# Kernel tuning notes

Measured on AMD Instinct MI355X. Metric: run time of the kernel, lower is better.

The kernel has to match this reference:

```python
import jax, jax.numpy as jnp
import numpy as np

B, H, W_, D, K = 64, 28, 28, 512, 32


def setup_inputs() -> dict:
    key = jax.random.key(0)
    k1, k2, k3 = jax.random.split(key, 3)
    x = jax.random.normal(k1, (B, H, W_, D), dtype=jnp.float32)
    # 1x1 conv weight, no bias: [D_in, K] (he_normal-like scale)
    W = jax.random.normal(k2, (D, K), dtype=jnp.float32) * np.sqrt(2.0 / D)
    # cluster offset tensor C (original shape (1,1,1,512,32), squeezed to [D,K])
    C = jax.random.normal(k3, (D, K), dtype=jnp.float32) * np.sqrt(2.0 / D)
    return {"x": x, "W": W, "C": C}


def reference(x, W, C):
    # 1x1 conv == per-pixel matmul: [B,H,W,D] @ [D,K] -> [B,H,W,K]
    s = jnp.einsum('bhwd,dk->bhwk', x, W)
    a = jax.nn.softmax(s, axis=-1)  # soft cluster assignment
    # Original math: v[b,d,k] = sum_{h,w} a[b,h,w,k] * (x[b,h,w,d] + C[d,k])
    # Algebraically identical split avoids the [B,H,W,D,K] 5D intermediate:
    #   sum_hw a*x  (matmul of assignments with features)
    # + (sum_hw a) * C  (cheap correction term)
    v = jnp.einsum('bhwk,bhwd->bdk', a, x) + jnp.sum(a, axis=(1, 2))[:, None, :] * C[None]
    return v.reshape(v.shape[0], -1)  # flatten -> [B, D*K]
```

## Files before the change

kernel.cpp:

```cpp
#include <hip/hip_runtime.h>

#define NB 64
#define HW 784
#define DD 512
#define KK 32
#define BPB 14
#define PPB 56
#define CHUNK 32
#define NCHUNK 2

typedef __attribute__((ext_vector_type(8))) short bf16x8;
typedef __attribute__((ext_vector_type(4))) float f32x4;

#define PART_F   ((size_t)NB * BPB * 4 * 16 * 64 * 4)
#define ASUM_OFF PART_F
#define WS_NEED  ((PART_F + (size_t)NB * BPB * KK) * sizeof(float))

__device__ __forceinline__ unsigned short f2bf(float f) {
    unsigned u = __float_as_uint(f);
    u += 0x7fffu + ((u >> 16) & 1u);
    return (unsigned short)(u >> 16);
}

template <bool USE_WS>
__global__ __launch_bounds__(256, 2) void netvlad_stage1(
    const float* __restrict__ x, const float* __restrict__ Wg,
    const float* __restrict__ Cg, float* __restrict__ out,
    float* __restrict__ ws)
{
    __shared__ __align__(16) unsigned short xs[CHUNK * 520];
    __shared__ float spart[4][CHUNK][33];
    __shared__ __align__(16) unsigned short aTe[KK * 40];
    __shared__ float ared[8][KK];
    __shared__ float asumF[KK];

    const int tid = threadIdx.x;
    const int l   = tid & 63, w = tid >> 6;
    const int l15 = l & 15,  lq = l >> 4;
    const int k   = tid & 31, pg = tid >> 5;
    const int bid = blockIdx.x;
    const int b   = bid / BPB;
    const int pb  = (bid % BPB) * PPB;
    const float* xb = x + (size_t)b * HW * DD;

    bf16x8 Wf[4][2];
#pragma unroll
    for (int ks = 0; ks < 4; ++ks)
#pragma unroll
        for (int nt = 0; nt < 2; ++nt)
#pragma unroll
            for (int j = 0; j < 8; ++j)
                Wf[ks][nt][j] = (short)f2bf(Wg[(w*128 + ks*32 + lq*8 + j) * KK + nt*16 + l15]);

    f32x4 acc[2][8];
#pragma unroll
    for (int mt = 0; mt < 2; ++mt)
#pragma unroll
        for (int nt = 0; nt < 8; ++nt)
#pragma unroll
            for (int jj = 0; jj < 4; ++jj) acc[mt][nt][jj] = 0.f;
    float asum_part = 0.f;

    auto stageChunk = [&](int c) {
#pragma unroll
        for (int h = 0; h < 2; ++h) {
            float4 r[8];
#pragma unroll
            for (int j = 0; j < 8; ++j) {
                const int f = tid + 256*(h*8 + j), row = f >> 7, c4 = f & 127;
                const int p = c*CHUNK + row;
                const int gp = pb + (p < PPB ? p : PPB - 1);
                r[j] = *(const float4*)(xb + (size_t)gp * DD + c4*4);
            }
#pragma unroll
            for (int j = 0; j < 8; ++j) {
                const int f = tid + 256*(h*8 + j), row = f >> 7, c4 = f & 127;
                uint2 pk = make_uint2((unsigned)f2bf(r[j].x) | ((unsigned)f2bf(r[j].y) << 16),
                                      (unsigned)f2bf(r[j].z) | ((unsigned)f2bf(r[j].w) << 16));
                *(uint2*)&xs[row*520 + c4*4] = pk;
            }
        }
    };

    stageChunk(0);
    __syncthreads();

    for (int c = 0; c < NCHUNK; ++c) {
        f32x4 sp[2][2];
#pragma unroll
        for (int mt = 0; mt < 2; ++mt)
#pragma unroll
            for (int nt = 0; nt < 2; ++nt)
#pragma unroll
                for (int jj = 0; jj < 4; ++jj) sp[mt][nt][jj] = 0.f;
#pragma unroll
        for (int ks = 0; ks < 4; ++ks) {
            bf16x8 af[2];
#pragma unroll
            for (int mt = 0; mt < 2; ++mt)
                af[mt] = *(const bf16x8*)&xs[(mt*16 + l15)*520 + w*128 + ks*32 + lq*8];
#pragma unroll
            for (int mt = 0; mt < 2; ++mt)
#pragma unroll
                for (int nt = 0; nt < 2; ++nt)
                    sp[mt][nt] = __builtin_amdgcn_mfma_f32_16x16x32_bf16(
                        af[mt], Wf[ks][nt], sp[mt][nt], 0, 0, 0);
        }
#pragma unroll
        for (int mt = 0; mt < 2; ++mt)
#pragma unroll
            for (int nt = 0; nt < 2; ++nt)
#pragma unroll
                for (int jj = 0; jj < 4; ++jj)
                    spart[w][mt*16 + lq*4 + jj][nt*16 + l15] = sp[mt][nt][jj];
        __syncthreads();

        const int valid = (PPB - c*CHUNK < CHUNK) ? (PPB - c*CHUNK) : CHUNK;
#pragma unroll
        for (int i = 0; i < 4; ++i) {
            const int p = pg + 8*i;
            const float s = spart[0][p][k] + spart[1][p][k]
                          + spart[2][p][k] + spart[3][p][k];
            const float e = __expf(s);
            float su = e;
#pragma unroll
            for (int msk = 16; msk >= 1; msk >>= 1)
                su += __shfl_xor(su, msk);
            const float a = (p < valid) ? e / su : 0.f;
            asum_part += a;
            aTe[k*40 + p] = f2bf(a);
        }
        __syncthreads();

        bf16x8 afr[2];
#pragma unroll
        for (int mt = 0; mt < 2; ++mt)
            afr[mt] = *(const bf16x8*)&aTe[(mt*16 + l15)*40 + lq*8];
#pragma unroll
        for (int nt = 0; nt < 8; ++nt) {
            const int d = w*128 + nt*16 + l15;
            bf16x8 bfr;
#pragma unroll
            for (int j = 0; j < 8; ++j) {
                const int jj = (j + 2*lq) & 7;
                bfr[jj] = (short)xs[(lq*8 + jj)*520 + d];
            }
#pragma unroll
            for (int mt = 0; mt < 2; ++mt)
                acc[mt][nt] = __builtin_amdgcn_mfma_f32_16x16x32_bf16(
                    afr[mt], bfr, acc[mt][nt], 0, 0, 0);
        }
        __syncthreads();

        if (c + 1 < NCHUNK) {
            stageChunk(c + 1);
            __syncthreads();
        }
    }

    ared[pg][k] = asum_part;
    __syncthreads();
    if (tid < KK) {
        float s = 0.f;
#pragma unroll
        for (int g = 0; g < 8; ++g) s += ared[g][tid];
        if (USE_WS) ws[ASUM_OFF + (size_t)bid * KK + tid] = s;
        else        asumF[tid] = s;
    }

    if (USE_WS) {
        float4* o = (float4*)ws + ((size_t)bid * 4 + w) * (16 * 64);
#pragma unroll
        for (int mt = 0; mt < 2; ++mt)
#pragma unroll
            for (int nt = 0; nt < 8; ++nt)
                o[(mt*8 + nt)*64 + l] = make_float4(acc[mt][nt][0], acc[mt][nt][1],
                                                    acc[mt][nt][2], acc[mt][nt][3]);
    } else {
        __syncthreads();
        float* ob = out + (size_t)b * (DD * KK);
#pragma unroll
        for (int mt = 0; mt < 2; ++mt)
#pragma unroll
            for (int nt = 0; nt < 8; ++nt)
#pragma unroll
                for (int jj = 0; jj < 4; ++jj) {
                    const int kk = mt*16 + lq*4 + jj;
                    const int d  = w*128 + nt*16 + l15;
                    atomicAdd(&ob[d*KK + kk], acc[mt][nt][jj] + asumF[kk] * Cg[d*KK + kk]);
                }
    }
}

__global__ __launch_bounds__(256) void netvlad_stage2(
    const float* __restrict__ ws, const float* __restrict__ Cg,
    float* __restrict__ out)
{
    __shared__ float lds[128 * 33];
    __shared__ float asumT[KK];

    const int t = threadIdx.x;
    const int b = blockIdx.x >> 2;
    const int w = blockIdx.x & 3;

    if (t < KK) {
        float s = 0.f;
#pragma unroll
        for (int p = 0; p < BPB; ++p)
            s += ws[ASUM_OFF + (size_t)(b*BPB + p) * KK + t];
        asumT[t] = s;
    }

    const float4* wsp = (const float4*)ws;
    float4 v[4];
#pragma unroll
    for (int i = 0; i < 4; ++i) v[i] = make_float4(0.f, 0.f, 0.f, 0.f);
    for (int p = 0; p < BPB; ++p) {
        const size_t base = ((size_t)(b*BPB + p) * 4 + w) * (16 * 64);
#pragma unroll
        for (int i = 0; i < 4; ++i) {
            const float4 f4 = wsp[base + t + 256*i];
            v[i].x += f4.x; v[i].y += f4.y; v[i].z += f4.z; v[i].w += f4.w;
        }
    }
#pragma unroll
    for (int i = 0; i < 4; ++i) {
        const int flat = t + 256*i;
        const int f = flat >> 6, lane = flat & 63;
        const int mt = f >> 3, nt = f & 7;
        const int q = lane >> 4, r15 = lane & 15;
        const int dl = nt*16 + r15;
        const int kb = mt*16 + q*4;
        lds[dl*33 + kb + 0] = v[i].x;
        lds[dl*33 + kb + 1] = v[i].y;
        lds[dl*33 + kb + 2] = v[i].z;
        lds[dl*33 + kb + 3] = v[i].w;
    }
    __syncthreads();

    float* outw = out + (size_t)b * (DD*KK) + w * 128 * KK;
    const float* Cw = Cg + w * 128 * KK;
#pragma unroll
    for (int i = 0; i < 4; ++i) {
        const int o4 = t + 256*i;
        const int dl = o4 >> 3, kq = (o4 & 7) * 4;
        const float4 c4 = *(const float4*)&Cw[dl*KK + kq];
        float4 rr;
        rr.x = lds[dl*33 + kq + 0] + asumT[kq + 0] * c4.x;
        rr.y = lds[dl*33 + kq + 1] + asumT[kq + 1] * c4.y;
        rr.z = lds[dl*33 + kq + 2] + asumT[kq + 2] * c4.z;
        rr.w = lds[dl*33 + kq + 3] + asumT[kq + 3] * c4.w;
        ((float4*)outw)[o4] = rr;
    }
}

extern "C" void kernel_launch(void* const* d_in, const int* in_sizes, int n_in,
                              void* d_out, int out_size, void* d_ws, size_t ws_size,
                              hipStream_t stream) {
    const float* x = (const float*)d_in[0];
    const float* W = (const float*)d_in[1];
    const float* C = (const float*)d_in[2];
    float* out = (float*)d_out;

    if (ws_size >= WS_NEED) {
        float* ws = (float*)d_ws;
        netvlad_stage1<true><<<dim3(NB * BPB), dim3(256), 0, stream>>>(x, W, C, out, ws);
        netvlad_stage2<<<dim3(NB * 4), dim3(256), 0, stream>>>(ws, C, out);
    } else {
        hipMemsetAsync(out, 0, (size_t)out_size * sizeof(float), stream);
        netvlad_stage1<false><<<dim3(NB * BPB), dim3(256), 0, stream>>>(x, W, C, out, nullptr);
    }
}
```

Before: 58.12 us.

## Use single-chunk blocks of 28 pixels and store partials in bf16

```diff
diff --git a/kernel.cpp b/kernel.cpp
--- a/kernel.cpp
+++ b/kernel.cpp
@@ -4,34 +4,36 @@
 #define HW 784
 #define DD 512
 #define KK 32
-#define BPB 14
-#define PPB 56
-#define CHUNK 32
-#define NCHUNK 2
+#define BPB 28
+#define PPB 28
+#define SLOTS 32
 
 typedef __attribute__((ext_vector_type(8))) short bf16x8;
 typedef __attribute__((ext_vector_type(4))) float f32x4;
-
-#define PART_F   ((size_t)NB * BPB * 4 * 16 * 64 * 4)
-#define ASUM_OFF PART_F
-#define WS_NEED  ((PART_F + (size_t)NB * BPB * KK) * sizeof(float))
+typedef __attribute__((ext_vector_type(4))) unsigned short u16x4;
+
+#define NBLK (NB * BPB)
+#define PART_BYTES ((size_t)NBLK * 4 * 16 * 64 * 8)
+#define WS_NEED    (PART_BYTES + (size_t)NBLK * KK * 4)
 
 __device__ __forceinline__ unsigned short f2bf(float f) {
     unsigned u = __float_as_uint(f);
     u += 0x7fffu + ((u >> 16) & 1u);
     return (unsigned short)(u >> 16);
 }
+__device__ __forceinline__ float bf2f(unsigned short u) {
+    return __uint_as_float((unsigned)u << 16);
+}
 
 template <bool USE_WS>
-__global__ __launch_bounds__(256, 2) void netvlad_stage1(
+__global__ __launch_bounds__(256) void netvlad_stage1(
     const float* __restrict__ x, const float* __restrict__ Wg,
     const float* __restrict__ Cg, float* __restrict__ out,
-    float* __restrict__ ws)
+    void* __restrict__ ws)
 {
-    __shared__ __align__(16) unsigned short xs[CHUNK * 520];
-    __shared__ float spart[4][CHUNK][33];
+    __shared__ __align__(16) unsigned short xs[SLOTS * 520];
+    __shared__ unsigned short spart[4][SLOTS][33];
     __shared__ __align__(16) unsigned short aTe[KK * 40];
-    __shared__ float ared[8][KK];
     __shared__ float asumF[KK];
 
     const int tid = threadIdx.x;
@@ -61,31 +63,26 @@
             for (int jj = 0; jj < 4; ++jj) acc[mt][nt][jj] = 0.f;
     float asum_part = 0.f;
 
-    auto stageChunk = [&](int c) {
-#pragma unroll
-        for (int h = 0; h < 2; ++h) {
-            float4 r[8];
-#pragma unroll
-            for (int j = 0; j < 8; ++j) {
-                const int f = tid + 256*(h*8 + j), row = f >> 7, c4 = f & 127;
-                const int p = c*CHUNK + row;
-                const int gp = pb + (p < PPB ? p : PPB - 1);
-                r[j] = *(const float4*)(xb + (size_t)gp * DD + c4*4);
-            }
-#pragma unroll
-            for (int j = 0; j < 8; ++j) {
-                const int f = tid + 256*(h*8 + j), row = f >> 7, c4 = f & 127;
-                uint2 pk = make_uint2((unsigned)f2bf(r[j].x) | ((unsigned)f2bf(r[j].y) << 16),
-                                      (unsigned)f2bf(r[j].z) | ((unsigned)f2bf(r[j].w) << 16));
-                *(uint2*)&xs[row*520 + c4*4] = pk;
-            }
-        }
-    };
-
-    stageChunk(0);
-    __syncthreads();
-
-    for (int c = 0; c < NCHUNK; ++c) {
+#pragma unroll
+    for (int h = 0; h < 2; ++h) {
+        float4 r[8];
+#pragma unroll
+        for (int j = 0; j < 8; ++j) {
+            const int f = tid + 256*(h*8 + j), row = f >> 7, c4 = f & 127;
+            const int gp = pb + (row < PPB ? row : PPB - 1);
+            r[j] = *(const float4*)(xb + (size_t)gp * DD + c4*4);
+        }
+#pragma unroll
+        for (int j = 0; j < 8; ++j) {
+            const int f = tid + 256*(h*8 + j), row = f >> 7, c4 = f & 127;
+            uint2 pk = make_uint2((unsigned)f2bf(r[j].x) | ((unsigned)f2bf(r[j].y) << 16),
+                                  (unsigned)f2bf(r[j].z) | ((unsigned)f2bf(r[j].w) << 16));
+            *(uint2*)&xs[row*520 + c4*4] = pk;
+        }
+    }
+    __syncthreads();
+
+    {
         f32x4 sp[2][2];
 #pragma unroll
         for (int mt = 0; mt < 2; ++mt)
@@ -112,26 +109,27 @@
             for (int nt = 0; nt < 2; ++nt)
 #pragma unroll
                 for (int jj = 0; jj < 4; ++jj)
-                    spart[w][mt*16 + lq*4 + jj][nt*16 + l15] = sp[mt][nt][jj];
-        __syncthreads();
-
-        const int valid = (PPB - c*CHUNK < CHUNK) ? (PPB - c*CHUNK) : CHUNK;
-#pragma unroll
-        for (int i = 0; i < 4; ++i) {
-            const int p = pg + 8*i;
-            const float s = spart[0][p][k] + spart[1][p][k]
-                          + spart[2][p][k] + spart[3][p][k];
-            const float e = __expf(s);
-            float su = e;
-#pragma unroll
-            for (int msk = 16; msk >= 1; msk >>= 1)
-                su += __shfl_xor(su, msk);
-            const float a = (p < valid) ? e / su : 0.f;
-            asum_part += a;
-            aTe[k*40 + p] = f2bf(a);
-        }
-        __syncthreads();
-
+                    spart[w][mt*16 + lq*4 + jj][nt*16 + l15] = f2bf(sp[mt][nt][jj]);
+    }
+    __syncthreads();
+
+#pragma unroll
+    for (int i = 0; i < 4; ++i) {
+        const int p = pg + 8*i;
+        const float s = bf2f(spart[0][p][k]) + bf2f(spart[1][p][k])
+                      + bf2f(spart[2][p][k]) + bf2f(spart[3][p][k]);
+        const float e = __expf(s);
+        float su = e;
+#pragma unroll
+        for (int msk = 16; msk >= 1; msk >>= 1)
+            su += __shfl_xor(su, msk);
+        const float a = (p < PPB) ? e * __builtin_amdgcn_rcpf(su) : 0.f;
+        asum_part += a;
+        aTe[k*40 + p] = f2bf(a);
+    }
+    __syncthreads();
+
+    {
         bf16x8 afr[2];
 #pragma unroll
         for (int mt = 0; mt < 2; ++mt)
@@ -150,32 +148,32 @@
                 acc[mt][nt] = __builtin_amdgcn_mfma_f32_16x16x32_bf16(
                     afr[mt], bfr, acc[mt][nt], 0, 0, 0);
         }
-        __syncthreads();
-
-        if (c + 1 < NCHUNK) {
-            stageChunk(c + 1);
-            __syncthreads();
-        }
-    }
-
-    ared[pg][k] = asum_part;
-    __syncthreads();
+    }
+    __syncthreads();
+
+    float* ared = (float*)aTe;
+    ared[pg*KK + k] = asum_part;
+    __syncthreads();
+    float* wsA = (float*)((char*)ws + PART_BYTES);
     if (tid < KK) {
         float s = 0.f;
 #pragma unroll
-        for (int g = 0; g < 8; ++g) s += ared[g][tid];
-        if (USE_WS) ws[ASUM_OFF + (size_t)bid * KK + tid] = s;
+        for (int g = 0; g < 8; ++g) s += ared[g*KK + tid];
+        if (USE_WS) wsA[(size_t)bid * KK + tid] = s;
         else        asumF[tid] = s;
     }
 
     if (USE_WS) {
-        float4* o = (float4*)ws + ((size_t)bid * 4 + w) * (16 * 64);
-#pragma unroll
-        for (int mt = 0; mt < 2; ++mt)
-#pragma unroll
-            for (int nt = 0; nt < 8; ++nt)
-                o[(mt*8 + nt)*64 + l] = make_float4(acc[mt][nt][0], acc[mt][nt][1],
-                                                    acc[mt][nt][2], acc[mt][nt][3]);
+        u16x4* o = (u16x4*)ws + ((size_t)bid * 4 + w) * (16 * 64);
+#pragma unroll
+        for (int mt = 0; mt < 2; ++mt)
+#pragma unroll
+            for (int nt = 0; nt < 8; ++nt) {
+                u16x4 u;
+                u[0] = f2bf(acc[mt][nt][0]); u[1] = f2bf(acc[mt][nt][1]);
+                u[2] = f2bf(acc[mt][nt][2]); u[3] = f2bf(acc[mt][nt][3]);
+                o[(mt*8 + nt)*64 + l] = u;
+            }
     } else {
         __syncthreads();
         float* ob = out + (size_t)b * (DD * KK);
@@ -193,7 +191,7 @@
 }
 
 __global__ __launch_bounds__(256) void netvlad_stage2(
-    const float* __restrict__ ws, const float* __restrict__ Cg,
+    const void* __restrict__ ws, const float* __restrict__ Cg,
     float* __restrict__ out)
 {
     __shared__ float lds[128 * 33];
@@ -201,33 +199,35 @@
 
     const int t = threadIdx.x;
     const int b = blockIdx.x >> 2;
-    const int w = blockIdx.x & 3;
-
+    const int jsl = blockIdx.x & 3;
+
+    const float* wsA = (const float*)((const char*)ws + PART_BYTES);
     if (t < KK) {
         float s = 0.f;
 #pragma unroll
         for (int p = 0; p < BPB; ++p)
-            s += ws[ASUM_OFF + (size_t)(b*BPB + p) * KK + t];
+            s += wsA[(size_t)(b*BPB + p) * KK + t];
         asumT[t] = s;
     }
 
-    const float4* wsp = (const float4*)ws;
+    const u16x4* wsp = (const u16x4*)ws;
     float4 v[4];
 #pragma unroll
     for (int i = 0; i < 4; ++i) v[i] = make_float4(0.f, 0.f, 0.f, 0.f);
     for (int p = 0; p < BPB; ++p) {
-        const size_t base = ((size_t)(b*BPB + p) * 4 + w) * (16 * 64);
+        const size_t base = ((size_t)(b*BPB + p) * 4 + jsl) * (16 * 64);
 #pragma unroll
         for (int i = 0; i < 4; ++i) {
-            const float4 f4 = wsp[base + t + 256*i];
-            v[i].x += f4.x; v[i].y += f4.y; v[i].z += f4.z; v[i].w += f4.w;
+            const u16x4 u = wsp[base + t + 256*i];
+            v[i].x += bf2f(u[0]); v[i].y += bf2f(u[1]);
+            v[i].z += bf2f(u[2]); v[i].w += bf2f(u[3]);
         }
     }
 #pragma unroll
     for (int i = 0; i < 4; ++i) {
         const int flat = t + 256*i;
-        const int f = flat >> 6, lane = flat & 63;
-        const int mt = f >> 3, nt = f & 7;
+        const int fr = flat >> 6, lane = flat & 63;
+        const int mt = fr >> 3, nt = fr & 7;
         const int q = lane >> 4, r15 = lane & 15;
         const int dl = nt*16 + r15;
         const int kb = mt*16 + q*4;
@@ -238,8 +238,8 @@
     }
     __syncthreads();
 
-    float* outw = out + (size_t)b * (DD*KK) + w * 128 * KK;
-    const float* Cw = Cg + w * 128 * KK;
+    float* outw = out + (size_t)b * (DD*KK) + jsl * 128 * KK;
+    const float* Cw = Cg + jsl * 128 * KK;
 #pragma unroll
     for (int i = 0; i < 4; ++i) {
         const int o4 = t + 256*i;
@@ -263,11 +263,10 @@
     float* out = (float*)d_out;
 
     if (ws_size >= WS_NEED) {
-        float* ws = (float*)d_ws;
-        netvlad_stage1<true><<<dim3(NB * BPB), dim3(256), 0, stream>>>(x, W, C, out, ws);
-        netvlad_stage2<<<dim3(NB * 4), dim3(256), 0, stream>>>(ws, C, out);
+        netvlad_stage1<true><<<dim3(NBLK), dim3(256), 0, stream>>>(x, W, C, out, d_ws);
+        netvlad_stage2<<<dim3(NB * 4), dim3(256), 0, stream>>>(d_ws, C, out);
     } else {
         hipMemsetAsync(out, 0, (size_t)out_size * sizeof(float), stream);
-        netvlad_stage1<false><<<dim3(NB * BPB), dim3(256), 0, stream>>>(x, W, C, out, nullptr);
-    }
-}
+        netvlad_stage1<false><<<dim3(NBLK), dim3(256), 0, stream>>>(x, W, C, out, d_ws);
+    }
+}
```

Result: faster. 50.50 us (-13.1%).
